# Kernel tuning notes

Measured on AMD Instinct MI355X. Metric: run time of the kernel, lower is better.

The kernel has to match this reference:

```python
import jax, jax.numpy as jnp
import numpy as np
from jax import lax

NUM_CLASSES = 4   # includes ignore label 0
IGNORE = 0
MAX_SAMPLES = 1024
HALF = MAX_SAMPLES // 2
BIG = 1 << 30     # sentinel key for invalid/unselected pixels


def setup_inputs() -> dict:
    key = jax.random.key(0)
    k1, k2, k3 = jax.random.split(key, 3)
    B, C, H, W = 4, 64, 256, 256
    feat_map = jax.random.normal(k1, (B, C, H, W), dtype=jnp.float32)
    labels = jax.random.randint(k2, (B, H, W), 0, NUM_CLASSES, dtype=jnp.int32)
    preds = jax.random.normal(k3, (B, NUM_CLASSES, H, W), dtype=jnp.float32)
    return {"feat_map": feat_map, "labels": labels, "preds": preds}


def _soft_dilate2d(x):
    # F.max_pool2d(x, kernel=3, stride=1, padding=1) on [B,1,H,W]
    return lax.reduce_window(x, -jnp.inf, lax.max, (1, 1, 3, 3), (1, 1, 1, 1), "SAME")


def _per_pair(fm, lab, pd, cls):
    # fm: [C, N] features, lab: [N] int labels, pd: [N] dilated pred class, cls: scalar int
    N = lab.shape[0]
    ar = jnp.arange(N)
    clsf = cls.astype(pd.dtype)
    in_cls = lab == cls
    hard = (pd != clsf) & in_cls   # mispredicted (after dilation) pixels of this class
    easy = (pd == clsf) & in_cls
    # torch code uses randperm; reference uses the deterministic identity
    # permutation: keep the first HALF hard pixels (in raster order).
    hard_key = jnp.where(hard, ar, BIG)
    hard_top = jnp.sort(hard_key)[:HALF]                      # [HALF]
    valid_h = (hard_top < BIG).astype(fm.dtype)
    feat_h = fm[:, jnp.where(hard_top < BIG, hard_top, 0)] * valid_h  # [C, HALF], zero-padded
    # rest pool = leftover hard pixels (rank >= HALF) first, then easy pixels;
    # keep first HALF of that concatenation.
    hard_rank = jnp.cumsum(hard) - 1
    easy_rank = jnp.cumsum(easy) - 1
    excess = jnp.maximum(jnp.sum(hard) - HALF, 0)
    rest_key = jnp.where(hard & (hard_rank >= HALF), hard_rank - HALF,
                         jnp.where(easy, excess + easy_rank, BIG))
    order = jnp.argsort(rest_key)[:HALF]                      # pixel indices, valid first
    valid_r = (jnp.take(rest_key, order) < BIG).astype(fm.dtype)
    feat_r = fm[:, order] * valid_r                           # [C, HALF], zero-padded
    return jnp.concatenate([feat_h, feat_r], axis=1)          # [C, MAX_SAMPLES]


def reference(feat_map, labels, preds):
    B, C, H, W = feat_map.shape
    N = H * W
    # softmax preserves argmax -> skip the softmax
    pred_lab = jnp.argmax(preds, axis=1).astype(feat_map.dtype)[:, None]  # [B,1,H,W]
    preds_d = _soft_dilate2d(pred_lab).reshape(B, N)
    feat_flat = feat_map.reshape(B, C, N)
    lab_flat = labels.reshape(B, N)
    # assume all non-ignore classes present in each image (true w.h.p. for
    # random labels over 65536 pixels) -> static total_classes = B*(NUM_CLASSES-1)
    b_idx = jnp.repeat(jnp.arange(B), NUM_CLASSES - 1)
    cls_idx = jnp.tile(jnp.arange(1, NUM_CLASSES), B)
    feat_extract = jax.vmap(_per_pair)(feat_flat[b_idx], lab_flat[b_idx],
                                       preds_d[b_idx], cls_idx)  # [B*(NC-1), C, 1024]
    feat_label = cls_idx.astype(jnp.float32)
    return feat_extract, feat_label
```

## Files before the change

### kernel.cpp

```cpp
#include <hip/hip_runtime.h>

#define BB 4
#define CC 64
#define HH 256
#define WW 256
#define NPIX (HH*WW)
#define NCLS 4
#define NPAIR 12
#define HALF 512
#define MAXS 1024
#define NOUT (NPAIR*CC*MAXS)
#define NBAND 64
#define BANDPIX (NPIX/NBAND)


__global__ void __launch_bounds__(256) k_count(
        const float* __restrict__ preds, const int* __restrict__ labels,
        int* __restrict__ hardBuf, int* __restrict__ easyBuf,
        unsigned* __restrict__ bandCounts) {
    __shared__ unsigned char vm[4][WW];
    __shared__ unsigned short cnt[96];
    __shared__ unsigned short pre[96];
    int bx = blockIdx.x;
    int b = bx >> 6, band = bx & 63;
    int y0 = band * 4;
    int x = threadIdx.x;
    const float* pb = preds + (size_t)b * NCLS * NPIX;

    unsigned char am[6];
#pragma unroll
    for (int r = 0; r < 6; ++r) {
        int y = y0 + r - 1;
        unsigned char a = 0;
        if (y >= 0 && y < HH) {
            const float* p = pb + y * WW + x;
            float best = p[0];
            int arg = 0;
#pragma unroll
            for (int c = 1; c < NCLS; ++c) {
                float v = p[(size_t)c * NPIX];
                if (v > best) { best = v; arg = c; }
            }
            a = (unsigned char)arg;
        }
        am[r] = a;
    }
    unsigned char vmr[4];
#pragma unroll
    for (int ry = 0; ry < 4; ++ry) {
        int m = am[ry];
        if (am[ry + 1] > m) m = am[ry + 1];
        if (am[ry + 2] > m) m = am[ry + 2];
        vmr[ry] = (unsigned char)m;
        vm[ry][x] = (unsigned char)m;
    }
    __syncthreads();

    int lane = x & 63, w = x >> 6;
    unsigned long long lt = (1ull << lane) - 1ull;

    int labv[4], pos[4], cls4[4], typ4[4];
#pragma unroll
    for (int ry = 0; ry < 4; ++ry) {
        int m = vmr[ry];
        if (x > 0)      { int v = vm[ry][x - 1]; if (v > m) m = v; }
        if (x < WW - 1) { int v = vm[ry][x + 1]; if (v > m) m = v; }
        int l = labels[b * NPIX + (y0 + ry) * WW + x];
        labv[ry] = l;
        cls4[ry] = l - 1;
        typ4[ry] = (m == l) ? 1 : 0;
        int p = 0;
#pragma unroll
        for (int c = 1; c <= 3; ++c) {
            unsigned long long hm = __ballot(l == c && m != c);
            unsigned long long em = __ballot(l == c && m == c);
            if (lane == 0) {
                cnt[((c - 1) * 2 + 0) * 16 + ry * 4 + w] = (unsigned short)__popcll(hm);
                cnt[((c - 1) * 2 + 1) * 16 + ry * 4 + w] = (unsigned short)__popcll(em);
            }
            if (l == c) p = (int)__popcll(((m != c) ? hm : em) & lt);
        }
        pos[ry] = p;
    }
    __syncthreads();

    if (x < 96) {
        int base = x & ~15, k = x & 15;
        int s = 0;
        for (int j = 0; j < k; ++j) s += cnt[base + j];
        pre[x] = (unsigned short)s;
    }
    __syncthreads();

    if (x < 3) {
        int th = pre[(x * 2 + 0) * 16 + 15] + cnt[(x * 2 + 0) * 16 + 15];
        int te = pre[(x * 2 + 1) * 16 + 15] + cnt[(x * 2 + 1) * 16 + 15];
        bandCounts[(b * 3 + x) * NBAND + band] = (unsigned)th | ((unsigned)te << 16);
    }
#pragma unroll
    for (int ry = 0; ry < 4; ++ry) {
        int cc = cls4[ry];
        if (cc >= 0) {
            int c2 = cc * 2 + typ4[ry];
            int r = pre[c2 * 16 + ry * 4 + w] + pos[ry];
            int pair = b * 3 + cc;
            int* buf = typ4[ry] ? easyBuf : hardBuf;
            buf[(((pair << 6) | band) << 10) + r] = (y0 + ry) * WW + x;
        }
    }
}

__global__ void __launch_bounds__(256) k_gather(
        const float* __restrict__ feat, const int* __restrict__ hardBuf,
        const int* __restrict__ easyBuf, const unsigned* __restrict__ bandCounts,
        float* __restrict__ out) {
    __shared__ int cumH[NBAND + 1], cumE[NBAND + 1];
    int blk = blockIdx.x;
    int pc = blk >> 2;
    int q = blk & 3;
    int pair = pc >> 6, c = pc & 63;
    int t = threadIdx.x;
    if (t < NBAND) {
        unsigned v = bandCounts[pair * NBAND + t];
        int hv = (int)(v & 0xffffu), ev = (int)(v >> 16);
#pragma unroll
        for (int off = 1; off < 64; off <<= 1) {
            int hu = __shfl_up(hv, off, 64);
            int eu = __shfl_up(ev, off, 64);
            if (t >= off) { hv += hu; ev += eu; }
        }
        cumH[t + 1] = hv;
        cumE[t + 1] = ev;
        if (t == 0) { cumH[0] = 0; cumE[0] = 0; }
    }
    __syncthreads();

    int Nh = cumH[NBAND], Ne = cumE[NBAND];
    int excess = Nh - HALF; if (excess < 0) excess = 0;
    int hardEnd = Nh < MAXS ? Nh : MAXS;
    int easyStart = HALF + excess;
    int easyEnd = easyStart + Ne; if (easyEnd > MAXS) easyEnd = MAXS;
    if (c == 0 && q == 0 && t == 0)
        out[NOUT + pair] = (float)(pair % 3 + 1);

    int b = pair / 3;
    const float* fp = feat + (size_t)(b * CC + c) * NPIX;
    int s = q * 256 + t;
    bool isH = s < hardEnd;
    bool isE = (s >= easyStart) & (s < easyEnd);
    float val = 0.0f;
    if (isH | isE) {
        int r = isH ? s : s - easyStart;
        const int* cum = isH ? cumH : cumE;
        int lo = 0, hi = NBAND;
#pragma unroll
        for (int it = 0; it < 6; ++it) {
            int mid = (lo + hi) >> 1;
            if (cum[mid] <= r) lo = mid; else hi = mid;
        }
        int off = r - cum[lo];
        const int* buf = isH ? hardBuf : easyBuf;
        int pix = buf[(((pair << 6) | lo) << 10) + off];
        val = fp[pix];
    }
    out[blk * 256 + t] = val;
}

extern "C" void kernel_launch(void* const* d_in, const int* in_sizes, int n_in,
                              void* d_out, int out_size, void* d_ws, size_t ws_size,
                              hipStream_t stream) {
    const float* feat   = (const float*)d_in[0];
    const int*   labels = (const int*)d_in[1];
    const float* preds  = (const float*)d_in[2];
    float* out = (float*)d_out;

    int* hardBuf = (int*)d_ws;
    int* easyBuf = hardBuf + NPAIR * NBAND * 1024;
    unsigned* bandCounts = (unsigned*)(easyBuf + NPAIR * NBAND * 1024);

    k_count<<<NBAND * BB, 256, 0, stream>>>(preds, labels, hardBuf, easyBuf, bandCounts);
    k_gather<<<NPAIR * CC * 4, 256, 0, stream>>>(feat, hardBuf, easyBuf, bandCounts, out);
}
```

Before: 102.0 us.

## Halve band height for more count blocks and replace binary search with slot table

The count kernel now processes 2-row bands, giving 512 blocks instead of 256. This spreads the argmax/dilate/compaction work over more CUs and lowers per-band buffer capacity. The gather kernel now does a two-wave prefix scan over 128 bands and fills a shared-memory table that maps each output slot to its band and offset. This replaces the per-thread binary search but adds a serial fill loop and an extra barrier per block. The gather kernel has many more blocks than the count kernel, so that added per-block overhead may cancel the saving.

```diff
diff --git a/kernel.cpp b/kernel.cpp
--- a/kernel.cpp
+++ b/kernel.cpp
@@ -10,26 +10,26 @@
 #define HALF 512
 #define MAXS 1024
 #define NOUT (NPAIR*CC*MAXS)
-#define NBAND 64
-#define BANDPIX (NPIX/NBAND)
+#define NBAND 128
+#define BANDCAP 512
 
 
 __global__ void __launch_bounds__(256) k_count(
         const float* __restrict__ preds, const int* __restrict__ labels,
         int* __restrict__ hardBuf, int* __restrict__ easyBuf,
         unsigned* __restrict__ bandCounts) {
-    __shared__ unsigned char vm[4][WW];
-    __shared__ unsigned short cnt[96];
-    __shared__ unsigned short pre[96];
+    __shared__ unsigned char vm[2][WW];
+    __shared__ unsigned short cnt[48];
+    __shared__ unsigned short pre[48];
     int bx = blockIdx.x;
-    int b = bx >> 6, band = bx & 63;
-    int y0 = band * 4;
+    int b = bx >> 7, band = bx & 127;
+    int y0 = band * 2;
     int x = threadIdx.x;
     const float* pb = preds + (size_t)b * NCLS * NPIX;
 
-    unsigned char am[6];
-#pragma unroll
-    for (int r = 0; r < 6; ++r) {
+    unsigned char am[4];
+#pragma unroll
+    for (int r = 0; r < 4; ++r) {
         int y = y0 + r - 1;
         unsigned char a = 0;
         if (y >= 0 && y < HH) {
@@ -45,9 +45,9 @@
         }
         am[r] = a;
     }
-    unsigned char vmr[4];
-#pragma unroll
-    for (int ry = 0; ry < 4; ++ry) {
+    unsigned char vmr[2];
+#pragma unroll
+    for (int ry = 0; ry < 2; ++ry) {
         int m = am[ry];
         if (am[ry + 1] > m) m = am[ry + 1];
         if (am[ry + 2] > m) m = am[ry + 2];
@@ -59,24 +59,23 @@
     int lane = x & 63, w = x >> 6;
     unsigned long long lt = (1ull << lane) - 1ull;
 
-    int labv[4], pos[4], cls4[4], typ4[4];
-#pragma unroll
-    for (int ry = 0; ry < 4; ++ry) {
+    int pos[2], cls2[2], typ2[2];
+#pragma unroll
+    for (int ry = 0; ry < 2; ++ry) {
         int m = vmr[ry];
         if (x > 0)      { int v = vm[ry][x - 1]; if (v > m) m = v; }
         if (x < WW - 1) { int v = vm[ry][x + 1]; if (v > m) m = v; }
         int l = labels[b * NPIX + (y0 + ry) * WW + x];
-        labv[ry] = l;
-        cls4[ry] = l - 1;
-        typ4[ry] = (m == l) ? 1 : 0;
+        cls2[ry] = l - 1;
+        typ2[ry] = (m == l) ? 1 : 0;
         int p = 0;
 #pragma unroll
         for (int c = 1; c <= 3; ++c) {
             unsigned long long hm = __ballot(l == c && m != c);
             unsigned long long em = __ballot(l == c && m == c);
             if (lane == 0) {
-                cnt[((c - 1) * 2 + 0) * 16 + ry * 4 + w] = (unsigned short)__popcll(hm);
-                cnt[((c - 1) * 2 + 1) * 16 + ry * 4 + w] = (unsigned short)__popcll(em);
+                cnt[((c - 1) * 2 + 0) * 8 + ry * 4 + w] = (unsigned short)__popcll(hm);
+                cnt[((c - 1) * 2 + 1) * 8 + ry * 4 + w] = (unsigned short)__popcll(em);
             }
             if (l == c) p = (int)__popcll(((m != c) ? hm : em) & lt);
         }
@@ -84,8 +83,8 @@
     }
     __syncthreads();
 
-    if (x < 96) {
-        int base = x & ~15, k = x & 15;
+    if (x < 48) {
+        int base = x & ~7, k = x & 7;
         int s = 0;
         for (int j = 0; j < k; ++j) s += cnt[base + j];
         pre[x] = (unsigned short)s;
@@ -93,19 +92,19 @@
     __syncthreads();
 
     if (x < 3) {
-        int th = pre[(x * 2 + 0) * 16 + 15] + cnt[(x * 2 + 0) * 16 + 15];
-        int te = pre[(x * 2 + 1) * 16 + 15] + cnt[(x * 2 + 1) * 16 + 15];
+        int th = pre[(x * 2 + 0) * 8 + 7] + cnt[(x * 2 + 0) * 8 + 7];
+        int te = pre[(x * 2 + 1) * 8 + 7] + cnt[(x * 2 + 1) * 8 + 7];
         bandCounts[(b * 3 + x) * NBAND + band] = (unsigned)th | ((unsigned)te << 16);
     }
 #pragma unroll
-    for (int ry = 0; ry < 4; ++ry) {
-        int cc = cls4[ry];
+    for (int ry = 0; ry < 2; ++ry) {
+        int cc = cls2[ry];
         if (cc >= 0) {
-            int c2 = cc * 2 + typ4[ry];
-            int r = pre[c2 * 16 + ry * 4 + w] + pos[ry];
+            int c2 = cc * 2 + typ2[ry];
+            int r = pre[c2 * 8 + ry * 4 + w] + pos[ry];
             int pair = b * 3 + cc;
-            int* buf = typ4[ry] ? easyBuf : hardBuf;
-            buf[(((pair << 6) | band) << 10) + r] = (y0 + ry) * WW + x;
+            int* buf = typ2[ry] ? easyBuf : hardBuf;
+            buf[(((pair << 7) | band) << 9) + r] = (y0 + ry) * WW + x;
         }
     }
 }
@@ -115,20 +114,31 @@
         const int* __restrict__ easyBuf, const unsigned* __restrict__ bandCounts,
         float* __restrict__ out) {
     __shared__ int cumH[NBAND + 1], cumE[NBAND + 1];
+    __shared__ int wtotH, wtotE;
+    __shared__ unsigned tbl[256];
     int blk = blockIdx.x;
     int pc = blk >> 2;
     int q = blk & 3;
     int pair = pc >> 6, c = pc & 63;
     int t = threadIdx.x;
+    int lane = t & 63;
+
+    tbl[t] = 0xffffffffu;
+    int hv = 0, ev = 0;
     if (t < NBAND) {
         unsigned v = bandCounts[pair * NBAND + t];
-        int hv = (int)(v & 0xffffu), ev = (int)(v >> 16);
+        hv = (int)(v & 0xffffu); ev = (int)(v >> 16);
 #pragma unroll
         for (int off = 1; off < 64; off <<= 1) {
             int hu = __shfl_up(hv, off, 64);
             int eu = __shfl_up(ev, off, 64);
-            if (t >= off) { hv += hu; ev += eu; }
-        }
+            if (lane >= off) { hv += hu; ev += eu; }
+        }
+        if (t == 63) { wtotH = hv; wtotE = ev; }
+    }
+    __syncthreads();
+    if (t < NBAND) {
+        if (t >= 64) { hv += wtotH; ev += wtotE; }
         cumH[t + 1] = hv;
         cumE[t + 1] = ev;
         if (t == 0) { cumH[0] = 0; cumE[0] = 0; }
@@ -143,24 +153,33 @@
     if (c == 0 && q == 0 && t == 0)
         out[NOUT + pair] = (float)(pair % 3 + 1);
 
+    int qlo = q * 256, qhi = qlo + 256;
+    if (t < NBAND) {
+        int s0 = cumH[t], s1 = cumH[t + 1];
+        if (s1 > hardEnd) s1 = hardEnd;
+        if (s0 < qlo) s0 = qlo;
+        if (s1 > qhi) s1 = qhi;
+        unsigned entH = ((unsigned)t << 16) | (unsigned)cumH[t];
+        for (int s = s0; s < s1; ++s) tbl[s - qlo] = entH;
+        int e0 = easyStart + cumE[t], e1 = easyStart + cumE[t + 1];
+        if (e1 > easyEnd) e1 = easyEnd;
+        if (e0 < qlo) e0 = qlo;
+        if (e1 > qhi) e1 = qhi;
+        unsigned entE = 0x80000000u | ((unsigned)t << 16) |
+                        (unsigned)(easyStart + cumE[t]);
+        for (int s = e0; s < e1; ++s) tbl[s - qlo] = entE;
+    }
+    __syncthreads();
+
     int b = pair / 3;
     const float* fp = feat + (size_t)(b * CC + c) * NPIX;
-    int s = q * 256 + t;
-    bool isH = s < hardEnd;
-    bool isE = (s >= easyStart) & (s < easyEnd);
+    unsigned ent = tbl[t];
     float val = 0.0f;
-    if (isH | isE) {
-        int r = isH ? s : s - easyStart;
-        const int* cum = isH ? cumH : cumE;
-        int lo = 0, hi = NBAND;
-#pragma unroll
-        for (int it = 0; it < 6; ++it) {
-            int mid = (lo + hi) >> 1;
-            if (cum[mid] <= r) lo = mid; else hi = mid;
-        }
-        int off = r - cum[lo];
-        const int* buf = isH ? hardBuf : easyBuf;
-        int pix = buf[(((pair << 6) | lo) << 10) + off];
+    if (ent != 0xffffffffu) {
+        int band = (int)((ent >> 16) & 0xffu);
+        int off = (qlo + t) - (int)(ent & 0xffffu);
+        const int* buf = (ent & 0x80000000u) ? easyBuf : hardBuf;
+        int pix = buf[(((pair << 7) | band) << 9) + off];
         val = fp[pix];
     }
     out[blk * 256 + t] = val;
@@ -175,8 +194,8 @@
     float* out = (float*)d_out;
 
     int* hardBuf = (int*)d_ws;
-    int* easyBuf = hardBuf + NPAIR * NBAND * 1024;
-    unsigned* bandCounts = (unsigned*)(easyBuf + NPAIR * NBAND * 1024);
+    int* easyBuf = hardBuf + NPAIR * NBAND * BANDCAP;
+    unsigned* bandCounts = (unsigned*)(easyBuf + NPAIR * NBAND * BANDCAP);
 
     k_count<<<NBAND * BB, 256, 0, stream>>>(preds, labels, hardBuf, easyBuf, bandCounts);
     k_gather<<<NPAIR * CC * 4, 256, 0, stream>>>(feat, hardBuf, easyBuf, bandCounts, out);
```

Result: no change. 102.0 us (+0.0%).
